# Optimization experiments

Measured on AMD Instinct MI355X. Metric: run time of the kernel, lower is better.

The kernel has to match this reference:

```python
import jax, jax.numpy as jnp
import numpy as np
from jax import lax

M_DIM = 128
L1 = L2 = L3 = L4 = 4
L = L1 * L2 * L3 * L4  # 256
RANK = 2
BATCH, D = 4, 16
W = D - RANK + 1  # 15 windows per dim (linear mode, stride 1, drop)


def _make_bbasis():
    # Bbasis[idx, i] = prod_d cos(2*pi*(j_d+1)/(i+2)), idx = ((j1*L2+j2)*L3+j3)*L4+j4
    i = jnp.arange(M_DIM, dtype=jnp.float32)
    def c(Ld):
        j = jnp.arange(D_ := Ld, dtype=jnp.float32)
        return jnp.cos(2.0 * jnp.pi * (j[:, None] + 1.0) / (i[None, :] + 2.0))  # (Ld, m)
    B1, B2, B3, B4 = c(L1), c(L2), c(L3), c(L4)
    Bb = (B1[:, None, None, None, :] * B2[None, :, None, None, :]
          * B3[None, None, :, None, :] * B4[None, None, None, :, :])
    return Bb.reshape(L, M_DIM).astype(jnp.float32)


def setup_inputs() -> dict:
    key = jax.random.key(0)
    k1, k2, k3 = jax.random.split(key, 3)
    vec_arr = jax.random.normal(k1, (BATCH, D, D, D, D, M_DIM), dtype=jnp.float32)
    # M initialized as identity + small noise (nn.init.eye_ is exactly eye; noise keeps grads non-trivial)
    M = jnp.eye(M_DIM, dtype=jnp.float32) + 0.01 * jax.random.normal(k2, (M_DIM, M_DIM), dtype=jnp.float32)
    Acoeff = jax.random.uniform(k3, (M_DIM, L), minval=-0.1, maxval=0.1, dtype=jnp.float32)
    Bbasis = _make_bbasis()
    return {"vec_arr": vec_arr, "M": M, "Acoeff": Acoeff, "Bbasis": Bbasis}


def _basis_index():
    # window coords k_d in [0, W), basis index uses j_d = k_d mod L_d
    k = jnp.arange(W)
    j1 = (k % L1)[:, None, None, None]
    j2 = (k % L2)[None, :, None, None]
    j3 = (k % L3)[None, None, :, None]
    j4 = (k % L4)[None, None, None, :]
    idx = ((j1 * L2 + j2) * L3 + j3) * L4 + j4  # (W,W,W,W)
    return idx.reshape(-1)  # (W^4,)


def reference(vec_arr, M, Acoeff, Bbasis):
    # 4D sliding-window mean (linear mode, stride 1, 'drop'), rank_op='avg'.
    # mean(window @ M.T) == mean(window) @ M.T (linearity), so pool then one GEMM.
    win = (1, RANK, RANK, RANK, RANK, 1)
    pooled = lax.reduce_window(vec_arr, jnp.float32(0.0), lax.add, win,
                               (1, 1, 1, 1, 1, 1), 'VALID') / float(RANK ** 4)
    # agg[b, k1..k4, j] = sum_i pooled[...,i] * M[j,i]  (i.e. x @ M.T)
    agg = jnp.einsum('bwxyzi,ji->bwxyzj', pooled, M)  # (B, W,W,W,W, m)
    agg = agg.reshape(agg.shape[0], -1, M_DIM)        # (B, W^4, m)
    idx = _basis_index()                               # (W^4,)
    # Position-dependent descriptor N(k) = Acoeff[:, idx] * Bbasis[idx, :]
    Nk = Acoeff.T[idx] * Bbasis[idx]                   # (W^4, m)
    return Nk[None, :, :] - agg                        # (B, W^4, m) deviation
```

## Files before the change

### kernel.cpp

```cpp
#include <hip/hip_runtime.h>
#include <hip/hip_bf16.h>
#include <stdint.h>

#define MD   128
#define LBAS 256

#define MBF_OFF 131072ull
#define WS_NEED (131072ull + 32768ull)

typedef __attribute__((ext_vector_type(8))) __bf16 bf16x8;
typedef __attribute__((ext_vector_type(4))) float floatx4;
typedef __attribute__((ext_vector_type(8))) unsigned short ushortx8;
typedef __attribute__((ext_vector_type(4))) unsigned short ushortx4;

__device__ __forceinline__ float bf2f(unsigned short u){
  union { unsigned int i; float f; } v; v.i = ((unsigned int)u) << 16; return v.f;
}
__device__ __forceinline__ unsigned short f2bf(float x){
  union { float f; unsigned int i; } v; v.f = x;
  unsigned int r = v.i + 0x7FFFu + ((v.i >> 16) & 1u);
  return (unsigned short)(r >> 16);
}
__device__ __forceinline__ int detect_f32(const void* Bbasis){
  return ((const unsigned int*)Bbasis)[0] == 0x3F800000u;
}

__global__ __launch_bounds__(256) void nk2_kernel(const void* __restrict__ Acoeff,
                                                  const void* __restrict__ Bbasis,
                                                  const void* __restrict__ Mmat,
                                                  float* __restrict__ NkFull,
                                                  unsigned short* __restrict__ Mbf){
  int gid = blockIdx.x * 256 + threadIdx.x;
  const int isf = detect_f32(Bbasis);
  if (gid < LBAS * MD){
    int idx = gid >> 7, j = gid & 127;
    float a, b;
    if (isf){ a = ((const float*)Acoeff)[j*LBAS+idx]; b = ((const float*)Bbasis)[idx*MD+j]; }
    else    { a = bf2f(((const unsigned short*)Acoeff)[j*LBAS+idx]);
              b = bf2f(((const unsigned short*)Bbasis)[idx*MD+j]); }
    NkFull[gid] = a * b;
  } else {
    int m = gid - LBAS * MD;
    if (m < MD * MD){
      Mbf[m] = isf ? f2bf(((const float*)Mmat)[m]) : ((const unsigned short*)Mmat)[m];
    }
  }
}

__global__ __launch_bounds__(256, 4) void mega_kernel(const void* __restrict__ vec,
                                                      const float* __restrict__ NkFull,
                                                      const unsigned short* __restrict__ Mbf,
                                                      const void* __restrict__ Bbasis,
                                                      void* __restrict__ out){
  __shared__ __align__(16) float S[32 * 132];
  __shared__ __align__(16) unsigned short Ab[16 * 136];
  __shared__ __align__(16) float sNk[16 * 128];

  const int xcd  = blockIdx.x & 7;
  const int slot = blockIdx.x >> 3;
  const int b    = xcd >> 1;
  const int s    = slot * 2 + (xcd & 1);
  if (s >= 225) return;
  const int w3 = s / 15;
  const int w2 = s - w3 * 15;
  const int t  = threadIdx.x;
  const int isf = detect_f32(Bbasis);

  const int wave = t >> 6, lane = t & 63;
  const int quad = lane >> 4, l16 = lane & 15;

  const size_t vbase0 = (size_t)b * 8388608 + (size_t)w2 * 32768 + (size_t)w3 * 2048;

  int offF[4];
#pragma unroll
  for (int k = 0; k < 4; ++k){
    const int ci = k * 256 + t;
    const int row = ci >> 5;
    offF[k] = (row >> 4) * 2048 + (row & 15) * 128 + (ci & 31) * 4;
  }
  int offB[2];
#pragma unroll
  for (int k = 0; k < 2; ++k){
    const int ci = k * 256 + t;
    const int row = ci >> 4;
    offB[k] = (row >> 4) * 2048 + (row & 15) * 128 + (ci & 15) * 8;
  }

  floatx4 pre[4][2];

  if (isf){
    const float* vf = (const float*)vec + vbase0;
#pragma unroll
    for (int k = 0; k < 4; ++k){
      pre[k][0] = *(const floatx4*)(vf + offF[k]);
      pre[k][1] = *(const floatx4*)(vf + offF[k] + 32768);
    }
  } else {
    const unsigned short* vh = (const unsigned short*)vec + vbase0;
#pragma unroll
    for (int k = 0; k < 2; ++k){
      *(ushortx8*)&pre[k][0] = *(const ushortx8*)(vh + offB[k]);
      *(ushortx8*)&pre[k][1] = *(const ushortx8*)(vh + offB[k] + 32768);
    }
  }

  bf16x8 mfr[2][4];
#pragma unroll
  for (int cc = 0; cc < 2; ++cc)
#pragma unroll
    for (int s4 = 0; s4 < 4; ++s4)
      *(ushortx8*)&mfr[cc][s4] =
          *(const ushortx8*)(Mbf + ((wave * 2 + cc) * 16 + l16) * 128 + s4 * 32 + quad * 8);

  {
    const int j2f = (w2 & 3), j3f = (w3 & 3);
#pragma unroll
    for (int k = 0; k < 2; ++k){
      const int ci = k * 256 + t;
      const int row16 = ci >> 5, c4 = (ci & 31) * 4;
      const int j1 = row16 >> 2, j4 = row16 & 3;
      const int nkrow = ((j1 * 4 + j2f) * 4 + j3f) * 4 + j4;
      *(floatx4*)&sNk[row16 * 128 + c4] = *(const floatx4*)&NkFull[nkrow * 128 + c4];
    }
    if (t >= 240){
      const ushortx8 z = (ushortx8){0,0,0,0,0,0,0,0};
      *(ushortx8*)&Ab[15 * 136 + (t & 15) * 8] = z;
    }
  }

  const int pw4 = t >> 4;
  const int pc8 = (t & 15) * 8;
  const int owner = (t < 240);
  float prv[8];

  for (int x1 = 0; x1 < 16; ++x1){
    if (isf){
#pragma unroll
      for (int k = 0; k < 4; ++k){
        const int ci = k * 256 + t;
        const int row = ci >> 5, c4 = (ci & 31) * 4;
        floatx4 sv;
#pragma unroll
        for (int q = 0; q < 4; ++q) sv[q] = pre[k][0][q] + pre[k][1][q];
        *(floatx4*)&S[row * 132 + c4] = sv;
      }
    } else {
#pragma unroll
      for (int k = 0; k < 2; ++k){
        const int ci = k * 256 + t;
        const int row = ci >> 4, c8 = (ci & 15) * 8;
        const ushortx8 a = *(const ushortx8*)&pre[k][0];
        const ushortx8 c = *(const ushortx8*)&pre[k][1];
#pragma unroll
        for (int q = 0; q < 8; ++q) S[row * 132 + c8 + q] = bf2f(a[q]) + bf2f(c[q]);
      }
    }

    if (x1 < 15){
      if (isf){
        const float* vf = (const float*)vec + vbase0 + (size_t)(x1 + 1) * 524288;
#pragma unroll
        for (int k = 0; k < 4; ++k){
          pre[k][0] = *(const floatx4*)(vf + offF[k]);
          pre[k][1] = *(const floatx4*)(vf + offF[k] + 32768);
        }
      } else {
        const unsigned short* vh = (const unsigned short*)vec + vbase0 + (size_t)(x1 + 1) * 524288;
#pragma unroll
        for (int k = 0; k < 2; ++k){
          *(ushortx8*)&pre[k][0] = *(const ushortx8*)(vh + offB[k]);
          *(ushortx8*)&pre[k][1] = *(const ushortx8*)(vh + offB[k] + 32768);
        }
      }
    }
    __syncthreads();

    if (owner){
      const int p0 = pw4 * 132 + pc8;
      const floatx4 a0 = *(const floatx4*)&S[p0];
      const floatx4 a1 = *(const floatx4*)&S[p0 + 4];
      const floatx4 b0 = *(const floatx4*)&S[p0 + 132];
      const floatx4 b1 = *(const floatx4*)&S[p0 + 136];
      const floatx4 c0 = *(const floatx4*)&S[p0 + 16 * 132];
      const floatx4 c1 = *(const floatx4*)&S[p0 + 16 * 132 + 4];
      const floatx4 d0 = *(const floatx4*)&S[p0 + 17 * 132];
      const floatx4 d1 = *(const floatx4*)&S[p0 + 17 * 132 + 4];
      float cur[8];
      const floatx4 lo = ((a0 + b0) + (c0 + d0)) * 0.125f;
      const floatx4 hi = ((a1 + b1) + (c1 + d1)) * 0.125f;
#pragma unroll
      for (int e = 0; e < 4; ++e){ cur[e] = lo[e]; cur[4 + e] = hi[e]; }
      if (x1 > 0){
        ushortx8 av;
#pragma unroll
        for (int e = 0; e < 8; ++e) av[e] = f2bf((cur[e] + prv[e]) * 0.5f);
        *(ushortx8*)&Ab[pw4 * 136 + pc8] = av;
      }
#pragma unroll
      for (int e = 0; e < 8; ++e) prv[e] = cur[e];
    }
    __syncthreads();

    if (x1 > 0){
      floatx4 acc[2];
      acc[0] = (floatx4){0.f,0.f,0.f,0.f};
      acc[1] = (floatx4){0.f,0.f,0.f,0.f};
#pragma unroll
      for (int s4 = 0; s4 < 4; ++s4){
        const bf16x8 af = *(const bf16x8*)&Ab[l16 * 136 + s4 * 32 + quad * 8];
#pragma unroll
        for (int cc = 0; cc < 2; ++cc){
          acc[cc] = __builtin_amdgcn_mfma_f32_16x16x32_bf16(mfr[cc][s4], af, acc[cc], 0, 0, 0);
        }
      }

      if (l16 < 15){
        const int w1 = x1 - 1;
        const int j1sel = w1 & 3;
        const size_t outBase = ((size_t)(((b * 15 + w1) * 15 + w2) * 15 + w3)) * 15;
        const size_t rowOff = (outBase + l16) * 128;
        const int nkRow = (j1sel * 4 + (l16 & 3)) * 128;
#pragma unroll
        for (int cc = 0; cc < 2; ++cc){
          const int col = (wave * 2 + cc) * 16 + quad * 4;
          const floatx4 nk = *(const floatx4*)&sNk[nkRow + col];
          floatx4 o;
#pragma unroll
          for (int e = 0; e < 4; ++e) o[e] = nk[e] - acc[cc][e];
          if (isf){
            *(floatx4*)((float*)out + rowOff + col) = o;
          } else {
            ushortx4 ob;
#pragma unroll
            for (int e = 0; e < 4; ++e) ob[e] = f2bf(o[e]);
            *(ushortx4*)((unsigned short*)out + rowOff + col) = ob;
          }
        }
      }
    }
  }
}

extern "C" void kernel_launch(void* const* d_in, const int* in_sizes, int n_in,
                              void* d_out, int out_size, void* d_ws, size_t ws_size,
                              hipStream_t stream) {
  const void* vec = d_in[0];
  const void* Mm  = d_in[1];
  const void* Ac  = d_in[2];
  const void* Bb  = d_in[3];

  float* NkFull = (float*)d_ws;
  unsigned short* Mbf = (unsigned short*)((char*)d_ws + MBF_OFF);

  nk2_kernel<<<192, 256, 0, stream>>>(Ac, Bb, Mm, NkFull, Mbf);
  mega_kernel<<<904, 256, 0, stream>>>(vec, NkFull, Mbf, Bb, d_out);
}
```

Baseline: 259.3 us.

## Stage MFMA output through LDS for coalesced row-contiguous stores; use lighter barriers

Swaps the MFMA operand order so the accumulator is laid out by output row, writes the results into a new LDS tile, then lets all 256 threads emit contiguous 16-byte row stores with the Nk subtraction. This is meant to replace the scattered per-lane 16-byte stores to 15 rows with coalesced writes. It adds an extra barrier and about 8 KB more LDS per block, which may reduce occupancy. The __syncthreads calls become a custom lgkmcnt wait plus s_barrier wrapped in sched barriers, which no longer waits on outstanding global loads.

```diff
diff --git a/kernel.cpp b/kernel.cpp
--- a/kernel.cpp
+++ b/kernel.cpp
@@ -23,6 +23,13 @@
 }
 __device__ __forceinline__ int detect_f32(const void* Bbasis){
   return ((const unsigned int*)Bbasis)[0] == 0x3F800000u;
+}
+
+__device__ __forceinline__ void bar_lgkm(){
+  __builtin_amdgcn_sched_barrier(0);
+  asm volatile("s_waitcnt lgkmcnt(0)" ::: "memory");
+  __builtin_amdgcn_s_barrier();
+  __builtin_amdgcn_sched_barrier(0);
 }
 
 __global__ __launch_bounds__(256) void nk2_kernel(const void* __restrict__ Acoeff,
@@ -53,6 +60,7 @@
                                                       const void* __restrict__ Bbasis,
                                                       void* __restrict__ out){
   __shared__ __align__(16) float S[32 * 132];
+  __shared__ __align__(16) float Ct[16 * 132];
   __shared__ __align__(16) unsigned short Ab[16 * 136];
   __shared__ __align__(16) float sNk[16 * 128];
 
@@ -173,7 +181,7 @@
         }
       }
     }
-    __syncthreads();
+    bar_lgkm();
 
     if (owner){
       const int p0 = pw4 * 132 + pc8;
@@ -199,7 +207,7 @@
 #pragma unroll
       for (int e = 0; e < 8; ++e) prv[e] = cur[e];
     }
-    __syncthreads();
+    bar_lgkm();
 
     if (x1 > 0){
       floatx4 acc[2];
@@ -210,30 +218,36 @@
         const bf16x8 af = *(const bf16x8*)&Ab[l16 * 136 + s4 * 32 + quad * 8];
 #pragma unroll
         for (int cc = 0; cc < 2; ++cc){
-          acc[cc] = __builtin_amdgcn_mfma_f32_16x16x32_bf16(mfr[cc][s4], af, acc[cc], 0, 0, 0);
-        }
-      }
-
-      if (l16 < 15){
-        const int w1 = x1 - 1;
-        const int j1sel = w1 & 3;
-        const size_t outBase = ((size_t)(((b * 15 + w1) * 15 + w2) * 15 + w3)) * 15;
-        const size_t rowOff = (outBase + l16) * 128;
-        const int nkRow = (j1sel * 4 + (l16 & 3)) * 128;
-#pragma unroll
-        for (int cc = 0; cc < 2; ++cc){
-          const int col = (wave * 2 + cc) * 16 + quad * 4;
-          const floatx4 nk = *(const floatx4*)&sNk[nkRow + col];
+          acc[cc] = __builtin_amdgcn_mfma_f32_16x16x32_bf16(af, mfr[cc][s4], acc[cc], 0, 0, 0);
+        }
+      }
+#pragma unroll
+      for (int cc = 0; cc < 2; ++cc)
+#pragma unroll
+        for (int reg = 0; reg < 4; ++reg)
+          Ct[(quad * 4 + reg) * 132 + (wave * 2 + cc) * 16 + l16] = acc[cc][reg];
+      bar_lgkm();
+
+      const int w1 = x1 - 1;
+      const int j1sel = w1 & 3;
+      const size_t outBase = ((size_t)(((b * 15 + w1) * 15 + w2) * 15 + w3)) * 15;
+#pragma unroll
+      for (int k = 0; k < 2; ++k){
+        const int ci = k * 256 + t;
+        if (ci < 480){
+          const int row = ci >> 5, c4 = (ci & 31) * 4;
+          const floatx4 v  = *(const floatx4*)&Ct[row * 132 + c4];
+          const floatx4 nk = *(const floatx4*)&sNk[(j1sel * 4 + (row & 3)) * 128 + c4];
           floatx4 o;
 #pragma unroll
-          for (int e = 0; e < 4; ++e) o[e] = nk[e] - acc[cc][e];
+          for (int e = 0; e < 4; ++e) o[e] = nk[e] - v[e];
           if (isf){
-            *(floatx4*)((float*)out + rowOff + col) = o;
+            *(floatx4*)((float*)out + (outBase + row) * 128 + c4) = o;
           } else {
             ushortx4 ob;
 #pragma unroll
             for (int e = 0; e < 4; ++e) ob[e] = f2bf(o[e]);
-            *(ushortx4*)((unsigned short*)out + rowOff + col) = ob;
+            *(ushortx4*)((unsigned short*)out + (outBase + row) * 128 + c4) = ob;
           }
         }
       }
```

Measured after the change: 259.7 us. No clear change (+0.1%).
